# Optimization experiments

Hardware: AMD Instinct MI355X
Metric: run time of the kernel (lower is better)

Reference implementation:

```python
import jax, jax.numpy as jnp
import numpy as np

B = 8388608  # batch

def setup_inputs() -> dict:
    key = jax.random.key(0)
    ks = jax.random.split(key, 7)
    x = jax.random.normal(ks[0], (B, 2), dtype=jnp.float32)
    # PyTorch Linear: y = x @ W.T + b, W shape [out, in]
    W1 = jax.random.normal(ks[1], (3, 2), dtype=jnp.float32) * 0.5
    b1 = jax.random.normal(ks[2], (3,), dtype=jnp.float32) * 0.1
    W2 = jax.random.normal(ks[3], (2, 3), dtype=jnp.float32) * 0.5
    b2 = jax.random.normal(ks[4], (2,), dtype=jnp.float32) * 0.1
    W3 = jax.random.normal(ks[5], (1, 2), dtype=jnp.float32) * 0.5
    b3 = jax.random.normal(ks[6], (1,), dtype=jnp.float32) * 0.1
    return {"x": x, "W1": W1, "b1": b1, "W2": W2, "b2": b2, "W3": W3, "b3": b3}

def reference(x, W1, b1, W2, b2, W3, b3):
    h1 = jax.nn.relu(x @ W1.T + b1)          # [B, 3]
    h2 = jax.nn.relu(h1 @ W2.T + b2)         # [B, 2]
    out = jax.nn.sigmoid((h2 @ W3.T + b3).squeeze(-1))  # [B]
    return (out, h1, h2)
```

## Files before the change

kernel.cpp:

```cpp
#include <hip/hip_runtime.h>
#include <math.h>


#define RPB 512

typedef float v4f __attribute__((ext_vector_type(4)));
typedef float v2f __attribute__((ext_vector_type(2)));

__global__ __launch_bounds__(256) void mlp321_kernel(
    const float* __restrict__ x,
    const float* __restrict__ W1, const float* __restrict__ b1,
    const float* __restrict__ W2, const float* __restrict__ b2,
    const float* __restrict__ W3, const float* __restrict__ b3,
    float* __restrict__ out_p, float* __restrict__ h1_p, float* __restrict__ h2_p,
    int nrows)
{
    __shared__ __align__(16) float s_h1[RPB * 3];
    __shared__ __align__(16) float s_h2[RPB * 2];
    __shared__ __align__(16) float s_out[RPB];

    const int tid = threadIdx.x;
    const size_t base = (size_t)blockIdx.x * RPB;

    float w1[6], w2[6], w3v[2], bb1[3], bb2[2], bb3;
#pragma unroll
    for (int i = 0; i < 6; ++i) w1[i] = W1[i];
#pragma unroll
    for (int i = 0; i < 3; ++i) bb1[i] = b1[i];
#pragma unroll
    for (int i = 0; i < 6; ++i) w2[i] = W2[i];
#pragma unroll
    for (int i = 0; i < 2; ++i) bb2[i] = b2[i];
    w3v[0] = W3[0]; w3v[1] = W3[1];
    bb3 = b3[0];

    const bool full = (base + RPB) <= (size_t)nrows;

    if (full) {
        const v4f* xv = reinterpret_cast<const v4f*>(x + base * 2);
        v4f xa = xv[tid];
        const float xr[2][2] = {{xa.x, xa.y}, {xa.z, xa.w}};
        float h1v[2][3], h2v[2][2], ov[2];
#pragma unroll
        for (int r = 0; r < 2; ++r) {
            const float x0 = xr[r][0], x1 = xr[r][1];
#pragma unroll
            for (int j = 0; j < 3; ++j) {
                float v = fmaf(x0, w1[j * 2 + 0], fmaf(x1, w1[j * 2 + 1], bb1[j]));
                h1v[r][j] = v > 0.f ? v : 0.f;
            }
#pragma unroll
            for (int k = 0; k < 2; ++k) {
                float v = bb2[k];
#pragma unroll
                for (int j = 0; j < 3; ++j) v = fmaf(h1v[r][j], w2[k * 3 + j], v);
                h2v[r][k] = v > 0.f ? v : 0.f;
            }
            const float z = fmaf(h2v[r][0], w3v[0], fmaf(h2v[r][1], w3v[1], bb3));
            ov[r] = __builtin_amdgcn_rcpf(1.f + __expf(-z));
        }

        v2f* h1w = reinterpret_cast<v2f*>(&s_h1[6 * tid]);
        h1w[0] = (v2f){h1v[0][0], h1v[0][1]};
        h1w[1] = (v2f){h1v[0][2], h1v[1][0]};
        h1w[2] = (v2f){h1v[1][1], h1v[1][2]};
        *reinterpret_cast<v4f*>(&s_h2[4 * tid]) =
            (v4f){h2v[0][0], h2v[0][1], h2v[1][0], h2v[1][1]};
        *reinterpret_cast<v2f*>(&s_out[2 * tid]) = (v2f){ov[0], ov[1]};

        __syncthreads();

        const v4f* so = reinterpret_cast<const v4f*>(s_out);
        const v4f* s1 = reinterpret_cast<const v4f*>(s_h1);
        const v4f* s2 = reinterpret_cast<const v4f*>(s_h2);
        v4f* po = reinterpret_cast<v4f*>(out_p + base);
        v4f* p1 = reinterpret_cast<v4f*>(h1_p + base * 3);
        v4f* p2 = reinterpret_cast<v4f*>(h2_p + base * 2);

        p1[tid] = s1[tid];
        p2[tid] = s2[tid];
        if (tid < 128) {
            p1[256 + tid] = s1[256 + tid];
        } else {
            po[tid - 128] = so[tid - 128];
        }
    } else {
        const int remain = (int)((size_t)nrows - base);
        for (int r = tid; r < remain; r += 256) {
            const size_t row = base + r;
            const float x0 = x[row * 2 + 0], x1 = x[row * 2 + 1];
            float h1v[3];
#pragma unroll
            for (int j = 0; j < 3; ++j) {
                float v = fmaf(x0, w1[j * 2 + 0], fmaf(x1, w1[j * 2 + 1], bb1[j]));
                h1v[j] = v > 0.f ? v : 0.f;
                h1_p[row * 3 + j] = h1v[j];
            }
            float h2v[2];
#pragma unroll
            for (int k = 0; k < 2; ++k) {
                float v = bb2[k];
#pragma unroll
                for (int j = 0; j < 3; ++j) v = fmaf(h1v[j], w2[k * 3 + j], v);
                h2v[k] = v > 0.f ? v : 0.f;
                h2_p[row * 2 + k] = h2v[k];
            }
            const float z = fmaf(h2v[0], w3v[0], fmaf(h2v[1], w3v[1], bb3));
            out_p[row] = __builtin_amdgcn_rcpf(1.f + __expf(-z));
        }
    }
}

extern "C" void kernel_launch(void* const* d_in, const int* in_sizes, int n_in,
                              void* d_out, int out_size, void* d_ws, size_t ws_size,
                              hipStream_t stream) {
    const float* x  = (const float*)d_in[0];
    const float* W1 = (const float*)d_in[1];
    const float* b1 = (const float*)d_in[2];
    const float* W2 = (const float*)d_in[3];
    const float* b2 = (const float*)d_in[4];
    const float* W3 = (const float*)d_in[5];
    const float* b3 = (const float*)d_in[6];

    const int B = in_sizes[0] / 2;
    float* out_p = (float*)d_out;
    float* h1_p  = out_p + (size_t)B;
    float* h2_p  = h1_p + (size_t)B * 3;

    const int blocks = (B + RPB - 1) / RPB;
    mlp321_kernel<<<blocks, 256, 0, stream>>>(x, W1, b1, W2, b2, W3, b3,
                                              out_p, h1_p, h2_p, B);
}
```

Baseline: 259.7 us.

## Use persistent grid-stride blocks with double-buffered LDS and next-chunk prefetch

Replaces the one-block-per-512-row-chunk launch with a grid capped at 2048 blocks that stride over chunks. The next chunk's input is loaded before the barrier, and the LDS staging buffers are double-buffered so the next iteration's writes do not collide with the current stores. The aim is to hide global load latency and amortize block launch and weight loads. The cost is fewer resident waves to hide memory latency and doubled LDS per block, which may reduce occupancy. The tail rows are handled by a single designated block.

After: 262.7 us. Within noise of the previous version (+1.2%).

```diff
diff --git a/kernel.cpp b/kernel.cpp
--- a/kernel.cpp
+++ b/kernel.cpp
@@ -3,6 +3,7 @@
 
 
 #define RPB 512
+#define NBLK 2048
 
 typedef float v4f __attribute__((ext_vector_type(4)));
 typedef float v2f __attribute__((ext_vector_type(2)));
@@ -15,12 +16,11 @@
     float* __restrict__ out_p, float* __restrict__ h1_p, float* __restrict__ h2_p,
     int nrows)
 {
-    __shared__ __align__(16) float s_h1[RPB * 3];
-    __shared__ __align__(16) float s_h2[RPB * 2];
-    __shared__ __align__(16) float s_out[RPB];
+    __shared__ __align__(16) float s_h1[2][RPB * 3];
+    __shared__ __align__(16) float s_h2[2][RPB * 2];
+    __shared__ __align__(16) float s_out[2][RPB];
 
     const int tid = threadIdx.x;
-    const size_t base = (size_t)blockIdx.x * RPB;
 
     float w1[6], w2[6], w3v[2], bb1[3], bb2[2], bb3;
 #pragma unroll
@@ -34,11 +34,16 @@
     w3v[0] = W3[0]; w3v[1] = W3[1];
     bb3 = b3[0];
 
-    const bool full = (base + RPB) <= (size_t)nrows;
+    const int nfull = nrows / RPB;
+    const int gsz = gridDim.x;
+    const v4f* xv = reinterpret_cast<const v4f*>(x);
 
-    if (full) {
-        const v4f* xv = reinterpret_cast<const v4f*>(x + base * 2);
-        v4f xa = xv[tid];
+    int c = blockIdx.x;
+    int buf = 0;
+    v4f xa = {0.f, 0.f, 0.f, 0.f};
+    if (c < nfull) xa = xv[(size_t)c * 256 + tid];
+
+    while (c < nfull) {
         const float xr[2][2] = {{xa.x, xa.y}, {xa.z, xa.w}};
         float h1v[2][3], h2v[2][2], ov[2];
 #pragma unroll
@@ -59,24 +64,27 @@
             const float z = fmaf(h2v[r][0], w3v[0], fmaf(h2v[r][1], w3v[1], bb3));
             ov[r] = __builtin_amdgcn_rcpf(1.f + __expf(-z));
         }
-
-        v2f* h1w = reinterpret_cast<v2f*>(&s_h1[6 * tid]);
+        v2f* h1w = reinterpret_cast<v2f*>(&s_h1[buf][6 * tid]);
         h1w[0] = (v2f){h1v[0][0], h1v[0][1]};
         h1w[1] = (v2f){h1v[0][2], h1v[1][0]};
         h1w[2] = (v2f){h1v[1][1], h1v[1][2]};
-        *reinterpret_cast<v4f*>(&s_h2[4 * tid]) =
+        *reinterpret_cast<v4f*>(&s_h2[buf][4 * tid]) =
             (v4f){h2v[0][0], h2v[0][1], h2v[1][0], h2v[1][1]};
-        *reinterpret_cast<v2f*>(&s_out[2 * tid]) = (v2f){ov[0], ov[1]};
+        *reinterpret_cast<v2f*>(&s_out[buf][2 * tid]) = (v2f){ov[0], ov[1]};
+
+        const int cn = c + gsz;
+        v4f xn = {0.f, 0.f, 0.f, 0.f};
+        if (cn < nfull) xn = xv[(size_t)cn * 256 + tid];
 
         __syncthreads();
 
-        const v4f* so = reinterpret_cast<const v4f*>(s_out);
-        const v4f* s1 = reinterpret_cast<const v4f*>(s_h1);
-        const v4f* s2 = reinterpret_cast<const v4f*>(s_h2);
+        const size_t base = (size_t)c * RPB;
+        const v4f* so = reinterpret_cast<const v4f*>(s_out[buf]);
+        const v4f* s1 = reinterpret_cast<const v4f*>(s_h1[buf]);
+        const v4f* s2 = reinterpret_cast<const v4f*>(s_h2[buf]);
         v4f* po = reinterpret_cast<v4f*>(out_p + base);
         v4f* p1 = reinterpret_cast<v4f*>(h1_p + base * 3);
         v4f* p2 = reinterpret_cast<v4f*>(h2_p + base * 2);
-
         p1[tid] = s1[tid];
         p2[tid] = s2[tid];
         if (tid < 128) {
@@ -84,10 +92,16 @@
         } else {
             po[tid - 128] = so[tid - 128];
         }
-    } else {
-        const int remain = (int)((size_t)nrows - base);
-        for (int r = tid; r < remain; r += 256) {
-            const size_t row = base + r;
+
+        xa = xn;
+        c = cn;
+        buf ^= 1;
+    }
+
+    const int tail = nrows - nfull * RPB;
+    if (tail && (int)blockIdx.x == (gsz ? (nfull % gsz) : 0)) {
+        for (int r = tid; r < tail; r += 256) {
+            const size_t row = (size_t)nfull * RPB + r;
             const float x0 = x[row * 2 + 0], x1 = x[row * 2 + 1];
             float h1v[3];
 #pragma unroll
@@ -127,7 +141,9 @@
     float* h1_p  = out_p + (size_t)B;
     float* h2_p  = h1_p + (size_t)B * 3;
 
-    const int blocks = (B + RPB - 1) / RPB;
+    const int nfull = B / RPB;
+    int blocks = nfull < NBLK ? nfull : NBLK;
+    if (blocks < 1) blocks = 1;
     mlp321_kernel<<<blocks, 256, 0, stream>>>(x, W1, b1, W2, b2, W3, b3,
                                               out_p, h1_p, h2_p, B);
 }
```
